# Performance work log

Hardware: AMD Instinct MI355X
Metric: run time of the kernel (lower is better)

Reference implementation:

```python
import jax, jax.numpy as jnp
import numpy as np

NEG_SLOPE = 0.2
STRONG_CONVEXITY = 0.5


def _scalar(x, Wq, Wl, bl, Wz, wz_out, wq_out, wl_out):
    # x: [B, D]; Wq/Wl: [L, H, D]; bl: [L, H]; Wz: [L-1, H, H]
    # Precompute all per-layer x-dependent terms in two batched einsums.
    qx = jnp.einsum('lhd,bd->lbh', Wq, x) ** 2          # [L, B, H]
    lx = jnp.einsum('lhd,bd->lbh', Wl, x) + bl[:, None, :]  # [L, B, H]
    z = jax.nn.leaky_relu(qx[0] + lx[0], negative_slope=NEG_SLOPE)

    def step(z, inputs):
        W, q, l = inputs
        z = jax.nn.leaky_relu(z @ W.T + q + l, negative_slope=NEG_SLOPE)
        return z, None

    z, _ = jax.lax.scan(step, z, (Wz, qx[1:], lx[1:]))
    # Final layer to scalar output (no bias on last wx_lin per torch code).
    out = z @ wz_out.T + (x @ wq_out.T) ** 2 + x @ wl_out.T  # [B, 1]
    return out


def setup_inputs() -> dict:
    key = jax.random.key(0)
    ks = jax.random.split(key, 8)
    B, D, H, L = 8192, 128, 512, 10
    f32 = jnp.float32
    x = jax.random.normal(ks[0], (B, D), f32)
    Wq = jax.random.normal(ks[1], (L, H, D), f32) * (1.0 / np.sqrt(D))
    Wl = jax.random.normal(ks[2], (L, H, D), f32) * (1.0 / np.sqrt(D))
    bl = jax.random.normal(ks[3], (L, H), f32) * 0.01
    # wz weights are kept non-negative in the original (clamp/exp init)
    Wz = jnp.abs(jax.random.normal(ks[4], (L - 1, H, H), f32)) * (1.0 / np.sqrt(H))
    wz_out = jnp.abs(jax.random.normal(ks[5], (1, H), f32)) * (1.0 / np.sqrt(H))
    wq_out = jax.random.normal(ks[6], (1, D), f32) * (1.0 / np.sqrt(D))
    wl_out = jax.random.normal(ks[7], (1, D), f32) * (1.0 / np.sqrt(D))
    return {"x": x, "Wq": Wq, "Wl": Wl, "bl": bl, "Wz": Wz,
            "wz_out": wz_out, "wq_out": wq_out, "wl_out": wl_out}


def reference(x, Wq, Wl, bl, Wz, wz_out, wq_out, wl_out):
    # forward = (1 - mu) * d(scalar)/dx + mu * x, with grad_outputs = ones
    def scalar_sum(xx):
        return jnp.sum(_scalar(xx, Wq, Wl, bl, Wz, wz_out, wq_out, wl_out))

    gx = jax.grad(scalar_sum)(x)  # per-sample gradient, [B, D]
    return (1.0 - STRONG_CONVEXITY) * gx + STRONG_CONVEXITY * x
```

## Files before the change

### kernel.cpp

```cpp
#include <hip/hip_runtime.h>


#define Bn 8192
#define Dn 128
#define Hn 512
#define Ln 10

constexpr float NS = 0.2f;

typedef __attribute__((ext_vector_type(8))) short short8;
typedef __attribute__((ext_vector_type(4))) float f32x4;

typedef const __attribute__((address_space(1))) void GV;
typedef __attribute__((address_space(3))) void LV;

__device__ __forceinline__ void gload16(const void* g, void* l) {
    __builtin_amdgcn_global_load_lds((GV*)g, (LV*)l, 16, 0, 0);
}

#define MFMA(acc, a, b) acc = __builtin_amdgcn_mfma_f32_16x16x32_bf16(a, b, acc, 0, 0, 0)

__device__ __forceinline__ unsigned short bf16_rne(float v) {
    unsigned u = __float_as_uint(v);
    u += 0x7FFFu + ((u >> 16) & 1u);
    return (unsigned short)(u >> 16);
}
__device__ __forceinline__ float bf2f(unsigned short h) {
    return __uint_as_float(((unsigned)h) << 16);
}
__device__ __forceinline__ void split2(float v, unsigned short& h, unsigned short& l) {
    h = bf16_rne(v);
    l = bf16_rne(v - bf2f(h));
}


__global__ __launch_bounds__(256) void split_flat(const float* __restrict__ in,
        unsigned short* __restrict__ hi, unsigned short* __restrict__ lo, int n4) {
    int i = blockIdx.x * 256 + threadIdx.x;
    if (i >= n4) return;
    float4 v = ((const float4*)in)[i];
    ushort4 h, l;
    split2(v.x, h.x, l.x);
    split2(v.y, h.y, l.y);
    split2(v.z, h.z, l.z);
    split2(v.w, h.w, l.w);
    ((ushort4*)hi)[i] = h;
    ((ushort4*)lo)[i] = l;
}

__global__ __launch_bounds__(256) void transpose_split(const float* __restrict__ in,
        unsigned short* __restrict__ hi, unsigned short* __restrict__ lo, int R, int C) {
    __shared__ float t[32][33];
    const size_t off = (size_t)blockIdx.z * R * C;
    const float* src = in + off;
    unsigned short* dh = hi + off;
    unsigned short* dl = lo + off;
    const int r0 = blockIdx.x * 32, c0 = blockIdx.y * 32;
    const int tr = threadIdx.x >> 5, tc = threadIdx.x & 31;
#pragma unroll
    for (int i = 0; i < 4; ++i)
        t[tr + 8 * i][tc] = src[(size_t)(r0 + tr + 8 * i) * C + c0 + tc];
    __syncthreads();
#pragma unroll
    for (int i = 0; i < 4; ++i) {
        float v = t[tc][tr + 8 * i];
        unsigned short h, l; split2(v, h, l);
        size_t o = (size_t)(c0 + tr + 8 * i) * R + r0 + tc;
        dh[o] = h; dl[o] = l;
    }
}


__global__ __launch_bounds__(256) void fwd_mfma(
    const unsigned short* __restrict__ xh, const unsigned short* __restrict__ xl,
    const unsigned short* __restrict__ zph, const unsigned short* __restrict__ zpl,
    const unsigned short* __restrict__ Wzh, const unsigned short* __restrict__ Wzl,
    const unsigned short* __restrict__ Wqh, const unsigned short* __restrict__ Wql,
    const unsigned short* __restrict__ Wlh, const unsigned short* __restrict__ Wll,
    const float* __restrict__ bl,
    unsigned short* __restrict__ zoh, unsigned short* __restrict__ zol,
    unsigned short* __restrict__ mask16, int hasZ)
{
    __shared__ __align__(16) char smem[32768];
    unsigned short* Ah  = (unsigned short*)smem;
    unsigned short* Al  = (unsigned short*)(smem + 8192);
    unsigned short* B0h = (unsigned short*)(smem + 16384);
    unsigned short* B0l = (unsigned short*)(smem + 20480);
    unsigned short* B1h = (unsigned short*)(smem + 24576);
    unsigned short* B1l = (unsigned short*)(smem + 28672);

    const int tid = threadIdx.x;
    const int w = tid >> 6, lane = tid & 63;
    const int lq = lane >> 4, lc = lane & 15;
    const int wm = (w & 1) * 64, wn = (w >> 1) * 32;
    const int row0 = blockIdx.x * 128, col0 = blockIdx.y * 64;
    const int sr = lane >> 2, sk = (lane & 3) * 8;

    f32x4 accz[4][2], accu[4][2], accv[4][2];
#pragma unroll
    for (int i = 0; i < 4; ++i)
#pragma unroll
        for (int j = 0; j < 2; ++j)
#pragma unroll
            for (int r = 0; r < 4; ++r) { accz[i][j][r] = 0.f; accu[i][j][r] = 0.f; accv[i][j][r] = 0.f; }

    if (hasZ) {
        for (int k0 = 0; k0 < Hn; k0 += 32) {
            __syncthreads();
            for (int c = w; c < 8; c += 4) {
                size_t go = (size_t)(row0 + c * 16 + sr) * Hn + k0 + sk;
                gload16(zph + go, Ah + c * 512);
                gload16(zpl + go, Al + c * 512);
            }
            {
                int c = w;
                size_t go = (size_t)(col0 + c * 16 + sr) * Hn + k0 + sk;
                gload16(Wzh + go, B0h + c * 512);
                gload16(Wzl + go, B0l + c * 512);
            }
            __syncthreads();
            short8 ah[4], al[4];
#pragma unroll
            for (int mt = 0; mt < 4; ++mt) {
                int ao = (wm + mt * 16 + lc) * 32 + lq * 8;
                ah[mt] = *(const short8*)(Ah + ao);
                al[mt] = *(const short8*)(Al + ao);
            }
#pragma unroll
            for (int nt = 0; nt < 2; ++nt) {
                int bo = (wn + nt * 16 + lc) * 32 + lq * 8;
                short8 bh = *(const short8*)(B0h + bo);
                short8 bv = *(const short8*)(B0l + bo);
#pragma unroll
                for (int mt = 0; mt < 4; ++mt) {
                    MFMA(accz[mt][nt], ah[mt], bh);
                    MFMA(accz[mt][nt], ah[mt], bv);
                    MFMA(accz[mt][nt], al[mt], bh);
                }
            }
        }
    }

    for (int k0 = 0; k0 < Dn; k0 += 32) {
        __syncthreads();
        for (int c = w; c < 8; c += 4) {
            size_t go = (size_t)(row0 + c * 16 + sr) * Dn + k0 + sk;
            gload16(xh + go, Ah + c * 512);
            gload16(xl + go, Al + c * 512);
        }
        {
            int c = w;
            size_t go = (size_t)(col0 + c * 16 + sr) * Dn + k0 + sk;
            gload16(Wqh + go, B0h + c * 512);
            gload16(Wql + go, B0l + c * 512);
            gload16(Wlh + go, B1h + c * 512);
            gload16(Wll + go, B1l + c * 512);
        }
        __syncthreads();
        short8 ah[4], al[4];
#pragma unroll
        for (int mt = 0; mt < 4; ++mt) {
            int ao = (wm + mt * 16 + lc) * 32 + lq * 8;
            ah[mt] = *(const short8*)(Ah + ao);
            al[mt] = *(const short8*)(Al + ao);
        }
#pragma unroll
        for (int nt = 0; nt < 2; ++nt) {
            int bo = (wn + nt * 16 + lc) * 32 + lq * 8;
            short8 bqh = *(const short8*)(B0h + bo);
            short8 bql = *(const short8*)(B0l + bo);
            short8 blh = *(const short8*)(B1h + bo);
            short8 bll = *(const short8*)(B1l + bo);
#pragma unroll
            for (int mt = 0; mt < 4; ++mt) {
                MFMA(accu[mt][nt], ah[mt], bqh);
                MFMA(accu[mt][nt], ah[mt], bql);
                MFMA(accu[mt][nt], al[mt], bqh);
                MFMA(accv[mt][nt], ah[mt], blh);
                MFMA(accv[mt][nt], ah[mt], bll);
                MFMA(accv[mt][nt], al[mt], blh);
            }
        }
    }

#pragma unroll
    for (int nt = 0; nt < 2; ++nt) {
        const int colb = col0 + wn + nt * 16;
        const int col = colb + lc;
        const float blv = bl[col];
#pragma unroll
        for (int mt = 0; mt < 4; ++mt) {
            const int rowb = row0 + wm + mt * 16;
#pragma unroll
            for (int r = 0; r < 4; ++r) {
                float uq = accu[mt][nt][r];
                float pre = accz[mt][nt][r] + uq * uq + accv[mt][nt][r] + blv;
                bool m = pre >= 0.f;
                unsigned long long bal = __ballot(m);
                if (lc == 0) {
                    int rw = rowb + lq * 4 + r;
                    mask16[(size_t)rw * 32 + (colb >> 4)] =
                        (unsigned short)((bal >> (lq * 16)) & 0xFFFFull);
                }
                float zv = m ? pre : NS * pre;
                unsigned short h, l; split2(zv, h, l);
                size_t o = (size_t)(rowb + lq * 4 + r) * Hn + col;
                zoh[o] = h; zol[o] = l;
            }
        }
    }
}


__global__ __launch_bounds__(256) void gemm_u_mfma(
    const unsigned short* __restrict__ xh, const unsigned short* __restrict__ xl,
    const unsigned short* __restrict__ Wqh, const unsigned short* __restrict__ Wql,
    float* __restrict__ u)
{
    __shared__ __align__(16) char smem[24576];
    unsigned short* Ah  = (unsigned short*)smem;
    unsigned short* Al  = (unsigned short*)(smem + 8192);
    unsigned short* B0h = (unsigned short*)(smem + 16384);
    unsigned short* B0l = (unsigned short*)(smem + 20480);

    const int tid = threadIdx.x;
    const int w = tid >> 6, lane = tid & 63;
    const int lq = lane >> 4, lc = lane & 15;
    const int wm = (w & 1) * 64, wn = (w >> 1) * 32;
    const int row0 = blockIdx.x * 128, col0 = blockIdx.y * 64;
    const int sr = lane >> 2, sk = (lane & 3) * 8;

    f32x4 acc[4][2];
#pragma unroll
    for (int i = 0; i < 4; ++i)
#pragma unroll
        for (int j = 0; j < 2; ++j)
#pragma unroll
            for (int r = 0; r < 4; ++r) acc[i][j][r] = 0.f;

    for (int k0 = 0; k0 < Dn; k0 += 32) {
        __syncthreads();
        for (int c = w; c < 8; c += 4) {
            size_t go = (size_t)(row0 + c * 16 + sr) * Dn + k0 + sk;
            gload16(xh + go, Ah + c * 512);
            gload16(xl + go, Al + c * 512);
        }
        {
            int c = w;
            size_t go = (size_t)(col0 + c * 16 + sr) * Dn + k0 + sk;
            gload16(Wqh + go, B0h + c * 512);
            gload16(Wql + go, B0l + c * 512);
        }
        __syncthreads();
        short8 ah[4], al[4];
#pragma unroll
        for (int mt = 0; mt < 4; ++mt) {
            int ao = (wm + mt * 16 + lc) * 32 + lq * 8;
            ah[mt] = *(const short8*)(Ah + ao);
            al[mt] = *(const short8*)(Al + ao);
        }
#pragma unroll
        for (int nt = 0; nt < 2; ++nt) {
            int bo = (wn + nt * 16 + lc) * 32 + lq * 8;
            short8 bh = *(const short8*)(B0h + bo);
            short8 bv = *(const short8*)(B0l + bo);
#pragma unroll
            for (int mt = 0; mt < 4; ++mt) {
                MFMA(acc[mt][nt], ah[mt], bh);
                MFMA(acc[mt][nt], ah[mt], bv);
                MFMA(acc[mt][nt], al[mt], bh);
            }
        }
    }

#pragma unroll
    for (int nt = 0; nt < 2; ++nt) {
        const int col = col0 + wn + nt * 16 + lc;
#pragma unroll
        for (int mt = 0; mt < 4; ++mt) {
            const int rowb = row0 + wm + mt * 16;
#pragma unroll
            for (int r = 0; r < 4; ++r)
                u[(size_t)(rowb + lq * 4 + r) * Hn + col] = acc[mt][nt][r];
        }
    }
}


__global__ __launch_bounds__(256) void bwd_g_mfma(
    const unsigned short* __restrict__ gah, const unsigned short* __restrict__ gal,
    const unsigned short* __restrict__ WzTh, const unsigned short* __restrict__ WzTl,
    const unsigned short* __restrict__ maskprev,
    unsigned short* __restrict__ goh, unsigned short* __restrict__ gol)
{
    __shared__ __align__(16) char smem[24576];
    unsigned short* Ah  = (unsigned short*)smem;
    unsigned short* Al  = (unsigned short*)(smem + 8192);
    unsigned short* B0h = (unsigned short*)(smem + 16384);
    unsigned short* B0l = (unsigned short*)(smem + 20480);

    const int tid = threadIdx.x;
    const int w = tid >> 6, lane = tid & 63;
    const int lq = lane >> 4, lc = lane & 15;
    const int wm = (w & 1) * 64, wn = (w >> 1) * 32;
    const int row0 = blockIdx.x * 128, col0 = blockIdx.y * 64;
    const int sr = lane >> 2, sk = (lane & 3) * 8;

    f32x4 acc[4][2];
#pragma unroll
    for (int i = 0; i < 4; ++i)
#pragma unroll
        for (int j = 0; j < 2; ++j)
#pragma unroll
            for (int r = 0; r < 4; ++r) acc[i][j][r] = 0.f;

    for (int k0 = 0; k0 < Hn; k0 += 32) {
        __syncthreads();
        for (int c = w; c < 8; c += 4) {
            size_t go = (size_t)(row0 + c * 16 + sr) * Hn + k0 + sk;
            gload16(gah + go, Ah + c * 512);
            gload16(gal + go, Al + c * 512);
        }
        {
            int c = w;
            size_t go = (size_t)(col0 + c * 16 + sr) * Hn + k0 + sk;
            gload16(WzTh + go, B0h + c * 512);
            gload16(WzTl + go, B0l + c * 512);
        }
        __syncthreads();
        short8 ah[4], al[4];
#pragma unroll
        for (int mt = 0; mt < 4; ++mt) {
            int ao = (wm + mt * 16 + lc) * 32 + lq * 8;
            ah[mt] = *(const short8*)(Ah + ao);
            al[mt] = *(const short8*)(Al + ao);
        }
#pragma unroll
        for (int nt = 0; nt < 2; ++nt) {
            int bo = (wn + nt * 16 + lc) * 32 + lq * 8;
            short8 bh = *(const short8*)(B0h + bo);
            short8 bv = *(const short8*)(B0l + bo);
#pragma unroll
            for (int mt = 0; mt < 4; ++mt) {
                MFMA(acc[mt][nt], ah[mt], bh);
                MFMA(acc[mt][nt], ah[mt], bv);
                MFMA(acc[mt][nt], al[mt], bh);
            }
        }
    }

#pragma unroll
    for (int nt = 0; nt < 2; ++nt) {
        const int colb = col0 + wn + nt * 16;
        const int col = colb + lc;
#pragma unroll
        for (int mt = 0; mt < 4; ++mt) {
            const int rowb = row0 + wm + mt * 16;
#pragma unroll
            for (int r = 0; r < 4; ++r) {
                int row = rowb + lq * 4 + r;
                unsigned short wbits = maskprev[(size_t)row * 32 + (colb >> 4)];
                float f = ((wbits >> lc) & 1) ? 1.f : NS;
                float v = acc[mt][nt][r] * f;
                unsigned short h, l; split2(v, h, l);
                size_t o = (size_t)row * Hn + col;
                goh[o] = h; gol[o] = l;
            }
        }
    }
}


__global__ __launch_bounds__(256) void bwd_x_mfma(
    const unsigned short* __restrict__ gah, const unsigned short* __restrict__ gal,
    const float* __restrict__ u,
    const unsigned short* __restrict__ WqTh, const unsigned short* __restrict__ WqTl,
    const unsigned short* __restrict__ WlTh, const unsigned short* __restrict__ WlTl,
    float* __restrict__ gx, int addTo)
{
    __shared__ __align__(16) char smem[32768];
    unsigned short* A1h = (unsigned short*)smem;
    unsigned short* A1l = (unsigned short*)(smem + 4096);
    unsigned short* A2h = (unsigned short*)(smem + 8192);
    unsigned short* A2l = (unsigned short*)(smem + 12288);
    unsigned short* Bqh = (unsigned short*)(smem + 16384);
    unsigned short* Bql = (unsigned short*)(smem + 20480);
    unsigned short* Blh = (unsigned short*)(smem + 24576);
    unsigned short* Bll = (unsigned short*)(smem + 28672);

    const int tid = threadIdx.x;
    const int w = tid >> 6, lane = tid & 63;
    const int lq = lane >> 4, lc = lane & 15;
    const int wm = (w & 1) * 32, wn = (w >> 1) * 32;
    const int row0 = blockIdx.x * 64, col0 = blockIdx.y * 64;
    const int sr = lane >> 2, sk = (lane & 3) * 8;
    const int ar = tid >> 2, as = (tid & 3) * 8;

    f32x4 acc[2][2];
#pragma unroll
    for (int i = 0; i < 2; ++i)
#pragma unroll
        for (int j = 0; j < 2; ++j)
#pragma unroll
            for (int r = 0; r < 4; ++r) acc[i][j][r] = 0.f;

    for (int k0 = 0; k0 < Hn; k0 += 32) {
        __syncthreads();
        {
            int c = w;
            size_t go = (size_t)(col0 + c * 16 + sr) * Hn + k0 + sk;
            gload16(WqTh + go, Bqh + c * 512);
            gload16(WqTl + go, Bql + c * 512);
            gload16(WlTh + go, Blh + c * 512);
            gload16(WlTl + go, Bll + c * 512);
        }
        {
            size_t gb = (size_t)(row0 + ar) * Hn + k0 + as;
            float4 u0 = *(const float4*)(u + gb);
            float4 u1 = *(const float4*)(u + gb + 4);
            ushort4 h0 = *(const ushort4*)(gah + gb);
            ushort4 h1 = *(const ushort4*)(gah + gb + 4);
            ushort4 l0 = *(const ushort4*)(gal + gb);
            ushort4 l1 = *(const ushort4*)(gal + gb + 4);
            int lo_ = ar * 32 + as;
            *(ushort4*)(A2h + lo_) = h0; *(ushort4*)(A2h + lo_ + 4) = h1;
            *(ushort4*)(A2l + lo_) = l0; *(ushort4*)(A2l + lo_ + 4) = l1;
            ushort4 oh, ol;
            float g, a1;
            g = bf2f(h0.x) + bf2f(l0.x); a1 = 2.f * u0.x * g; split2(a1, oh.x, ol.x);
            g = bf2f(h0.y) + bf2f(l0.y); a1 = 2.f * u0.y * g; split2(a1, oh.y, ol.y);
            g = bf2f(h0.z) + bf2f(l0.z); a1 = 2.f * u0.z * g; split2(a1, oh.z, ol.z);
            g = bf2f(h0.w) + bf2f(l0.w); a1 = 2.f * u0.w * g; split2(a1, oh.w, ol.w);
            *(ushort4*)(A1h + lo_) = oh; *(ushort4*)(A1l + lo_) = ol;
            g = bf2f(h1.x) + bf2f(l1.x); a1 = 2.f * u1.x * g; split2(a1, oh.x, ol.x);
            g = bf2f(h1.y) + bf2f(l1.y); a1 = 2.f * u1.y * g; split2(a1, oh.y, ol.y);
            g = bf2f(h1.z) + bf2f(l1.z); a1 = 2.f * u1.z * g; split2(a1, oh.z, ol.z);
            g = bf2f(h1.w) + bf2f(l1.w); a1 = 2.f * u1.w * g; split2(a1, oh.w, ol.w);
            *(ushort4*)(A1h + lo_ + 4) = oh; *(ushort4*)(A1l + lo_ + 4) = ol;
        }
        __syncthreads();
        short8 a1h[2], a1l[2], a2h[2], a2l[2];
#pragma unroll
        for (int mt = 0; mt < 2; ++mt) {
            int ao = (wm + mt * 16 + lc) * 32 + lq * 8;
            a1h[mt] = *(const short8*)(A1h + ao);
            a1l[mt] = *(const short8*)(A1l + ao);
            a2h[mt] = *(const short8*)(A2h + ao);
            a2l[mt] = *(const short8*)(A2l + ao);
        }
#pragma unroll
        for (int nt = 0; nt < 2; ++nt) {
            int bo = (wn + nt * 16 + lc) * 32 + lq * 8;
            short8 qh = *(const short8*)(Bqh + bo);
            short8 ql_ = *(const short8*)(Bql + bo);
            short8 lh = *(const short8*)(Blh + bo);
            short8 ll_ = *(const short8*)(Bll + bo);
#pragma unroll
            for (int mt = 0; mt < 2; ++mt) {
                MFMA(acc[mt][nt], a1h[mt], qh);
                MFMA(acc[mt][nt], a1h[mt], ql_);
                MFMA(acc[mt][nt], a1l[mt], qh);
                MFMA(acc[mt][nt], a2h[mt], lh);
                MFMA(acc[mt][nt], a2h[mt], ll_);
                MFMA(acc[mt][nt], a2l[mt], lh);
            }
        }
    }

#pragma unroll
    for (int nt = 0; nt < 2; ++nt) {
        const int col = col0 + wn + nt * 16 + lc;
#pragma unroll
        for (int mt = 0; mt < 2; ++mt) {
            const int rowb = row0 + wm + mt * 16;
#pragma unroll
            for (int r = 0; r < 4; ++r) {
                size_t o = (size_t)(rowb + lq * 4 + r) * Dn + col;
                float v = acc[mt][nt][r];
                if (addTo) v += gx[o];
                gx[o] = v;
            }
        }
    }
}


__global__ __launch_bounds__(256) void ga_init(
    const float* __restrict__ wz_out, const unsigned short* __restrict__ mask9,
    unsigned short* __restrict__ gh, unsigned short* __restrict__ gl)
{
    int i = blockIdx.x * 256 + threadIdx.x;
    int e = i << 2;
    int b = e >> 9, h = e & 511;
    unsigned short wbits = mask9[(size_t)b * 32 + (h >> 4)];
    float4 wv = *(const float4*)(wz_out + h);
    int sh = h & 15;
    ushort4 oh, ol;
    float f;
    f = wv.x * (((wbits >> (sh + 0)) & 1) ? 1.f : NS); split2(f, oh.x, ol.x);
    f = wv.y * (((wbits >> (sh + 1)) & 1) ? 1.f : NS); split2(f, oh.y, ol.y);
    f = wv.z * (((wbits >> (sh + 2)) & 1) ? 1.f : NS); split2(f, oh.z, ol.z);
    f = wv.w * (((wbits >> (sh + 3)) & 1) ? 1.f : NS); split2(f, oh.w, ol.w);
    *(ushort4*)(gh + e) = oh;
    *(ushort4*)(gl + e) = ol;
}

__global__ __launch_bounds__(256) void rowdot_kernel(
    const float* __restrict__ x, const float* __restrict__ wq_out, float* __restrict__ s) {
    const int b = blockIdx.x * 4 + (threadIdx.x >> 6);
    const int lane = threadIdx.x & 63;
    float v = x[(size_t)b * Dn + lane] * wq_out[lane] +
              x[(size_t)b * Dn + 64 + lane] * wq_out[64 + lane];
#pragma unroll
    for (int off = 32; off > 0; off >>= 1) v += __shfl_down(v, off, 64);
    if (lane == 0) s[b] = v;
}

__global__ __launch_bounds__(256) void final_kernel(
    float* __restrict__ out, const float* __restrict__ x, const float* __restrict__ s,
    const float* __restrict__ wq_out, const float* __restrict__ wl_out) {
    const int i = blockIdx.x * 256 + threadIdx.x;
    const int base = i << 2;
    const int b = base >> 7;
    const int d = base & (Dn - 1);
    float4 g = *(const float4*)(out + base);
    float4 xv = *(const float4*)(x + base);
    float4 wq = *(const float4*)(wq_out + d);
    float4 wl = *(const float4*)(wl_out + d);
    const float sb = s[b];
    float4 o;
    o.x = 0.5f * g.x + sb * wq.x + 0.5f * wl.x + 0.5f * xv.x;
    o.y = 0.5f * g.y + sb * wq.y + 0.5f * wl.y + 0.5f * xv.y;
    o.z = 0.5f * g.z + sb * wq.z + 0.5f * wl.z + 0.5f * xv.z;
    o.w = 0.5f * g.w + sb * wq.w + 0.5f * wl.w + 0.5f * xv.w;
    *(float4*)(out + base) = o;
}


extern "C" void kernel_launch(void* const* d_in, const int* in_sizes, int n_in,
                              void* d_out, int out_size, void* d_ws, size_t ws_size,
                              hipStream_t stream) {
    (void)in_sizes; (void)n_in; (void)out_size; (void)ws_size;
    const float* x      = (const float*)d_in[0];
    const float* Wq     = (const float*)d_in[1];
    const float* Wl     = (const float*)d_in[2];
    const float* bl     = (const float*)d_in[3];
    const float* Wz     = (const float*)d_in[4];
    const float* wz_out = (const float*)d_in[5];
    const float* wq_out = (const float*)d_in[6];
    const float* wl_out = (const float*)d_in[7];
    float* out = (float*)d_out;

    char* p = (char*)d_ws;
    #define CARVE(name, bytes) unsigned short* name = (unsigned short*)p; p += (((size_t)(bytes)) + 255) & ~(size_t)255;
    CARVE(xh,  (size_t)Bn*Dn*2)  CARVE(xl,  (size_t)Bn*Dn*2)
    CARVE(Wqh, (size_t)Ln*Hn*Dn*2) CARVE(Wql, (size_t)Ln*Hn*Dn*2)
    CARVE(Wlh, (size_t)Ln*Hn*Dn*2) CARVE(Wll, (size_t)Ln*Hn*Dn*2)
    CARVE(WqTh,(size_t)Ln*Hn*Dn*2) CARVE(WqTl,(size_t)Ln*Hn*Dn*2)
    CARVE(WlTh,(size_t)Ln*Hn*Dn*2) CARVE(WlTl,(size_t)Ln*Hn*Dn*2)
    CARVE(Wzh, (size_t)(Ln-1)*Hn*Hn*2) CARVE(Wzl, (size_t)(Ln-1)*Hn*Hn*2)
    CARVE(WzTh,(size_t)(Ln-1)*Hn*Hn*2) CARVE(WzTl,(size_t)(Ln-1)*Hn*Hn*2)
    CARVE(zAh, (size_t)Bn*Hn*2) CARVE(zAl, (size_t)Bn*Hn*2)
    CARVE(zBh, (size_t)Bn*Hn*2) CARVE(zBl, (size_t)Bn*Hn*2)
    float* uBuf = (float*)p; p += (size_t)Bn*Hn*4;
    float* s    = (float*)p; p += (size_t)Bn*4;
    unsigned short* mask16 = (unsigned short*)p; p += (size_t)Ln*Bn*32*2;
    #undef CARVE

    split_flat<<<(Bn*Dn/4 + 255)/256, 256, 0, stream>>>(x, xh, xl, Bn*Dn/4);
    split_flat<<<(Ln*Hn*Dn/4 + 255)/256, 256, 0, stream>>>(Wq, Wqh, Wql, Ln*Hn*Dn/4);
    split_flat<<<(Ln*Hn*Dn/4 + 255)/256, 256, 0, stream>>>(Wl, Wlh, Wll, Ln*Hn*Dn/4);
    split_flat<<<((Ln-1)*Hn*Hn/4 + 255)/256, 256, 0, stream>>>(Wz, Wzh, Wzl, (Ln-1)*Hn*Hn/4);
    transpose_split<<<dim3(Hn/32, Dn/32, Ln), 256, 0, stream>>>(Wq, WqTh, WqTl, Hn, Dn);
    transpose_split<<<dim3(Hn/32, Dn/32, Ln), 256, 0, stream>>>(Wl, WlTh, WlTl, Hn, Dn);
    transpose_split<<<dim3(Hn/32, Hn/32, Ln-1), 256, 0, stream>>>(Wz, WzTh, WzTl, Hn, Hn);

    rowdot_kernel<<<Bn/4, 256, 0, stream>>>(x, wq_out, s);

    const dim3 gF(Bn/128, Hn/64);

    fwd_mfma<<<gF, 256, 0, stream>>>(xh, xl, nullptr, nullptr, nullptr, nullptr,
        Wqh, Wql, Wlh, Wll, bl, zAh, zAl, mask16, 0);
    for (int l = 1; l < Ln; ++l) {
        const unsigned short* zh  = (l & 1) ? zAh : zBh;
        const unsigned short* zl_ = (l & 1) ? zAl : zBl;
        unsigned short* oh  = (l & 1) ? zBh : zAh;
        unsigned short* ol_ = (l & 1) ? zBl : zAl;
        fwd_mfma<<<gF, 256, 0, stream>>>(xh, xl, zh, zl_,
            Wzh + (size_t)(l-1)*Hn*Hn, Wzl + (size_t)(l-1)*Hn*Hn,
            Wqh + (size_t)l*Hn*Dn, Wql + (size_t)l*Hn*Dn,
            Wlh + (size_t)l*Hn*Dn, Wll + (size_t)l*Hn*Dn,
            bl + (size_t)l*Hn, oh, ol_, mask16 + (size_t)l*Bn*32, 1);
    }

    ga_init<<<(Bn*Hn/4)/256, 256, 0, stream>>>(wz_out, mask16 + (size_t)9*Bn*32, zAh, zAl);
    for (int l = Ln - 1; l >= 0; --l) {
        int sidx = (Ln - 1 - l) & 1;
        const unsigned short* gh_ = sidx ? zBh : zAh;
        const unsigned short* gl_ = sidx ? zBl : zAl;
        gemm_u_mfma<<<gF, 256, 0, stream>>>(xh, xl,
            Wqh + (size_t)l*Hn*Dn, Wql + (size_t)l*Hn*Dn, uBuf);
        bwd_x_mfma<<<dim3(Bn/64, Dn/64), 256, 0, stream>>>(gh_, gl_, uBuf,
            WqTh + (size_t)l*Dn*Hn, WqTl + (size_t)l*Dn*Hn,
            WlTh + (size_t)l*Dn*Hn, WlTl + (size_t)l*Dn*Hn,
            out, (l == Ln - 1) ? 0 : 1);
        if (l > 0) {
            unsigned short* oh  = sidx ? zAh : zBh;
            unsigned short* ol_ = sidx ? zAl : zBl;
            bwd_g_mfma<<<gF, 256, 0, stream>>>(gh_, gl_,
                WzTh + (size_t)(l-1)*Hn*Hn, WzTl + (size_t)(l-1)*Hn*Hn,
                mask16 + (size_t)(l-1)*Bn*32, oh, ol_);
        }
    }

    final_kernel<<<(Bn*Dn/4)/256, 256, 0, stream>>>(out, x, s, wq_out, wl_out);
}
```

Baseline: 928.4 us.

## Cache forward u, fuse backward g/x GEMMs into one launch, merge weight splits

The forward kernel now writes the pre-square Wq·x term u for every layer into a per-layer buffer. This removes the backward recomputation GEMM (gemm_u_mfma) at the cost of an extra Ln×B×H float buffer of writes and reads. The backward g-propagation and x-gradient GEMMs are merged into a single launch. Blocks are partitioned by index, so both run concurrently, and the x-gradient tile grows to 128 rows. The final elementwise combine is folded into the last backward epilogue, and the flat and transposed weight splits are produced by one kernel per weight.

```diff
diff --git a/kernel.cpp b/kernel.cpp
--- a/kernel.cpp
+++ b/kernel.cpp
@@ -48,18 +48,27 @@
     ((ushort4*)lo)[i] = l;
 }
 
-__global__ __launch_bounds__(256) void transpose_split(const float* __restrict__ in,
-        unsigned short* __restrict__ hi, unsigned short* __restrict__ lo, int R, int C) {
+__global__ __launch_bounds__(256) void split_both(const float* __restrict__ in,
+        unsigned short* __restrict__ hi, unsigned short* __restrict__ lo,
+        unsigned short* __restrict__ thi, unsigned short* __restrict__ tlo,
+        int R, int C) {
     __shared__ float t[32][33];
     const size_t off = (size_t)blockIdx.z * R * C;
     const float* src = in + off;
-    unsigned short* dh = hi + off;
-    unsigned short* dl = lo + off;
+    unsigned short* sh_ = hi + off;
+    unsigned short* sl_ = lo + off;
+    unsigned short* dh = thi + off;
+    unsigned short* dl = tlo + off;
     const int r0 = blockIdx.x * 32, c0 = blockIdx.y * 32;
     const int tr = threadIdx.x >> 5, tc = threadIdx.x & 31;
 #pragma unroll
-    for (int i = 0; i < 4; ++i)
-        t[tr + 8 * i][tc] = src[(size_t)(r0 + tr + 8 * i) * C + c0 + tc];
+    for (int i = 0; i < 4; ++i) {
+        size_t si = (size_t)(r0 + tr + 8 * i) * C + c0 + tc;
+        float v = src[si];
+        t[tr + 8 * i][tc] = v;
+        unsigned short h, l; split2(v, h, l);
+        sh_[si] = h; sl_[si] = l;
+    }
     __syncthreads();
 #pragma unroll
     for (int i = 0; i < 4; ++i) {
@@ -79,7 +88,7 @@
     const unsigned short* __restrict__ Wlh, const unsigned short* __restrict__ Wll,
     const float* __restrict__ bl,
     unsigned short* __restrict__ zoh, unsigned short* __restrict__ zol,
-    unsigned short* __restrict__ mask16, int hasZ)
+    unsigned short* __restrict__ mask16, float* __restrict__ uout, int hasZ)
 {
     __shared__ __align__(16) char smem[32768];
     unsigned short* Ah  = (unsigned short*)smem;
@@ -206,279 +215,207 @@
                 unsigned short h, l; split2(zv, h, l);
                 size_t o = (size_t)(rowb + lq * 4 + r) * Hn + col;
                 zoh[o] = h; zol[o] = l;
-            }
-        }
-    }
-}
-
-
-__global__ __launch_bounds__(256) void gemm_u_mfma(
-    const unsigned short* __restrict__ xh, const unsigned short* __restrict__ xl,
-    const unsigned short* __restrict__ Wqh, const unsigned short* __restrict__ Wql,
-    float* __restrict__ u)
+                uout[o] = uq;
+            }
+        }
+    }
+}
+
+
+__global__ __launch_bounds__(256) void bwd_combo(
+    const unsigned short* __restrict__ gah, const unsigned short* __restrict__ gal,
+    const unsigned short* __restrict__ WzTh, const unsigned short* __restrict__ WzTl,
+    const unsigned short* __restrict__ maskprev,
+    unsigned short* __restrict__ goh, unsigned short* __restrict__ gol,
+    const float* __restrict__ uL,
+    const unsigned short* __restrict__ WqTh, const unsigned short* __restrict__ WqTl,
+    const unsigned short* __restrict__ WlTh, const unsigned short* __restrict__ WlTl,
+    float* __restrict__ gx, int addTo, int nG, int finalF,
+    const float* __restrict__ xin, const float* __restrict__ s,
+    const float* __restrict__ wq_out, const float* __restrict__ wl_out)
 {
-    __shared__ __align__(16) char smem[24576];
-    unsigned short* Ah  = (unsigned short*)smem;
-    unsigned short* Al  = (unsigned short*)(smem + 8192);
-    unsigned short* B0h = (unsigned short*)(smem + 16384);
-    unsigned short* B0l = (unsigned short*)(smem + 20480);
-
+    __shared__ __align__(16) char smem[49152];
+    const int bid = blockIdx.x;
     const int tid = threadIdx.x;
     const int w = tid >> 6, lane = tid & 63;
     const int lq = lane >> 4, lc = lane & 15;
     const int wm = (w & 1) * 64, wn = (w >> 1) * 32;
-    const int row0 = blockIdx.x * 128, col0 = blockIdx.y * 64;
     const int sr = lane >> 2, sk = (lane & 3) * 8;
 
-    f32x4 acc[4][2];
-#pragma unroll
-    for (int i = 0; i < 4; ++i)
-#pragma unroll
-        for (int j = 0; j < 2; ++j)
-#pragma unroll
-            for (int r = 0; r < 4; ++r) acc[i][j][r] = 0.f;
-
-    for (int k0 = 0; k0 < Dn; k0 += 32) {
-        __syncthreads();
-        for (int c = w; c < 8; c += 4) {
-            size_t go = (size_t)(row0 + c * 16 + sr) * Dn + k0 + sk;
-            gload16(xh + go, Ah + c * 512);
-            gload16(xl + go, Al + c * 512);
-        }
-        {
-            int c = w;
-            size_t go = (size_t)(col0 + c * 16 + sr) * Dn + k0 + sk;
-            gload16(Wqh + go, B0h + c * 512);
-            gload16(Wql + go, B0l + c * 512);
-        }
-        __syncthreads();
-        short8 ah[4], al[4];
-#pragma unroll
-        for (int mt = 0; mt < 4; ++mt) {
-            int ao = (wm + mt * 16 + lc) * 32 + lq * 8;
-            ah[mt] = *(const short8*)(Ah + ao);
-            al[mt] = *(const short8*)(Al + ao);
-        }
+    if (bid < nG) {
+        unsigned short* Ah  = (unsigned short*)smem;
+        unsigned short* Al  = (unsigned short*)(smem + 8192);
+        unsigned short* B0h = (unsigned short*)(smem + 16384);
+        unsigned short* B0l = (unsigned short*)(smem + 20480);
+        const int row0 = (bid & 63) * 128, col0 = (bid >> 6) * 64;
+
+        f32x4 acc[4][2];
+#pragma unroll
+        for (int i = 0; i < 4; ++i)
+#pragma unroll
+            for (int j = 0; j < 2; ++j)
+#pragma unroll
+                for (int r = 0; r < 4; ++r) acc[i][j][r] = 0.f;
+
+        for (int k0 = 0; k0 < Hn; k0 += 32) {
+            __syncthreads();
+            for (int c = w; c < 8; c += 4) {
+                size_t go = (size_t)(row0 + c * 16 + sr) * Hn + k0 + sk;
+                gload16(gah + go, Ah + c * 512);
+                gload16(gal + go, Al + c * 512);
+            }
+            {
+                int c = w;
+                size_t go = (size_t)(col0 + c * 16 + sr) * Hn + k0 + sk;
+                gload16(WzTh + go, B0h + c * 512);
+                gload16(WzTl + go, B0l + c * 512);
+            }
+            __syncthreads();
+            short8 ah[4], al[4];
+#pragma unroll
+            for (int mt = 0; mt < 4; ++mt) {
+                int ao = (wm + mt * 16 + lc) * 32 + lq * 8;
+                ah[mt] = *(const short8*)(Ah + ao);
+                al[mt] = *(const short8*)(Al + ao);
+            }
+#pragma unroll
+            for (int nt = 0; nt < 2; ++nt) {
+                int bo = (wn + nt * 16 + lc) * 32 + lq * 8;
+                short8 bh = *(const short8*)(B0h + bo);
+                short8 bv = *(const short8*)(B0l + bo);
+#pragma unroll
+                for (int mt = 0; mt < 4; ++mt) {
+                    MFMA(acc[mt][nt], ah[mt], bh);
+                    MFMA(acc[mt][nt], ah[mt], bv);
+                    MFMA(acc[mt][nt], al[mt], bh);
+                }
+            }
+        }
+
 #pragma unroll
         for (int nt = 0; nt < 2; ++nt) {
-            int bo = (wn + nt * 16 + lc) * 32 + lq * 8;
-            short8 bh = *(const short8*)(B0h + bo);
-            short8 bv = *(const short8*)(B0l + bo);
+            const int colb = col0 + wn + nt * 16;
+            const int col = colb + lc;
 #pragma unroll
             for (int mt = 0; mt < 4; ++mt) {
-                MFMA(acc[mt][nt], ah[mt], bh);
-                MFMA(acc[mt][nt], ah[mt], bv);
-                MFMA(acc[mt][nt], al[mt], bh);
-            }
-        }
-    }
-
-#pragma unroll
-    for (int nt = 0; nt < 2; ++nt) {
-        const int col = col0 + wn + nt * 16 + lc;
-#pragma unroll
-        for (int mt = 0; mt < 4; ++mt) {
-            const int rowb = row0 + wm + mt * 16;
-#pragma unroll
-            for (int r = 0; r < 4; ++r)
-                u[(size_t)(rowb + lq * 4 + r) * Hn + col] = acc[mt][nt][r];
-        }
-    }
-}
-
-
-__global__ __launch_bounds__(256) void bwd_g_mfma(
-    const unsigned short* __restrict__ gah, const unsigned short* __restrict__ gal,
-    const unsigned short* __restrict__ WzTh, const unsigned short* __restrict__ WzTl,
-    const unsigned short* __restrict__ maskprev,
-    unsigned short* __restrict__ goh, unsigned short* __restrict__ gol)
-{
-    __shared__ __align__(16) char smem[24576];
-    unsigned short* Ah  = (unsigned short*)smem;
-    unsigned short* Al  = (unsigned short*)(smem + 8192);
-    unsigned short* B0h = (unsigned short*)(smem + 16384);
-    unsigned short* B0l = (unsigned short*)(smem + 20480);
-
-    const int tid = threadIdx.x;
-    const int w = tid >> 6, lane = tid & 63;
-    const int lq = lane >> 4, lc = lane & 15;
-    const int wm = (w & 1) * 64, wn = (w >> 1) * 32;
-    const int row0 = blockIdx.x * 128, col0 = blockIdx.y * 64;
-    const int sr = lane >> 2, sk = (lane & 3) * 8;
-
-    f32x4 acc[4][2];
-#pragma unroll
-    for (int i = 0; i < 4; ++i)
-#pragma unroll
-        for (int j = 0; j < 2; ++j)
-#pragma unroll
-            for (int r = 0; r < 4; ++r) acc[i][j][r] = 0.f;
-
-    for (int k0 = 0; k0 < Hn; k0 += 32) {
-        __syncthreads();
-        for (int c = w; c < 8; c += 4) {
-            size_t go = (size_t)(row0 + c * 16 + sr) * Hn + k0 + sk;
-            gload16(gah + go, Ah + c * 512);
-            gload16(gal + go, Al + c * 512);
-        }
-        {
-            int c = w;
-            size_t go = (size_t)(col0 + c * 16 + sr) * Hn + k0 + sk;
-            gload16(WzTh + go, B0h + c * 512);
-            gload16(WzTl + go, B0l + c * 512);
-        }
-        __syncthreads();
-        short8 ah[4], al[4];
-#pragma unroll
-        for (int mt = 0; mt < 4; ++mt) {
-            int ao = (wm + mt * 16 + lc) * 32 + lq * 8;
-            ah[mt] = *(const short8*)(Ah + ao);
-            al[mt] = *(const short8*)(Al + ao);
-        }
+                const int rowb = row0 + wm + mt * 16;
+#pragma unroll
+                for (int r = 0; r < 4; ++r) {
+                    int row = rowb + lq * 4 + r;
+                    unsigned short wbits = maskprev[(size_t)row * 32 + (colb >> 4)];
+                    float f = ((wbits >> lc) & 1) ? 1.f : NS;
+                    float v = acc[mt][nt][r] * f;
+                    unsigned short h, l; split2(v, h, l);
+                    size_t o = (size_t)row * Hn + col;
+                    goh[o] = h; gol[o] = l;
+                }
+            }
+        }
+    } else {
+        unsigned short* A1h = (unsigned short*)smem;
+        unsigned short* A1l = (unsigned short*)(smem + 8192);
+        unsigned short* A2h = (unsigned short*)(smem + 16384);
+        unsigned short* A2l = (unsigned short*)(smem + 24576);
+        unsigned short* Bqh = (unsigned short*)(smem + 32768);
+        unsigned short* Bql = (unsigned short*)(smem + 36864);
+        unsigned short* Blh = (unsigned short*)(smem + 40960);
+        unsigned short* Bll = (unsigned short*)(smem + 45056);
+
+        const int t = bid - nG;
+        const int row0 = (t >> 1) * 128, col0 = (t & 1) * 64;
+        const int ar = tid >> 2, as = (tid & 3) * 8;
+
+        f32x4 acc[4][2];
+#pragma unroll
+        for (int i = 0; i < 4; ++i)
+#pragma unroll
+            for (int j = 0; j < 2; ++j)
+#pragma unroll
+                for (int r = 0; r < 4; ++r) acc[i][j][r] = 0.f;
+
+        for (int k0 = 0; k0 < Hn; k0 += 32) {
+            __syncthreads();
+            {
+                int c = w;
+                size_t go = (size_t)(col0 + c * 16 + sr) * Hn + k0 + sk;
+                gload16(WqTh + go, Bqh + c * 512);
+                gload16(WqTl + go, Bql + c * 512);
+                gload16(WlTh + go, Blh + c * 512);
+                gload16(WlTl + go, Bll + c * 512);
+            }
+#pragma unroll
+            for (int rr = 0; rr < 2; ++rr) {
+                const int lr = rr * 64 + ar;
+                size_t gb = (size_t)(row0 + lr) * Hn + k0 + as;
+                float4 u0 = *(const float4*)(uL + gb);
+                float4 u1 = *(const float4*)(uL + gb + 4);
+                ushort4 h0 = *(const ushort4*)(gah + gb);
+                ushort4 h1 = *(const ushort4*)(gah + gb + 4);
+                ushort4 l0 = *(const ushort4*)(gal + gb);
+                ushort4 l1 = *(const ushort4*)(gal + gb + 4);
+                int lo_ = lr * 32 + as;
+                *(ushort4*)(A2h + lo_) = h0; *(ushort4*)(A2h + lo_ + 4) = h1;
+                *(ushort4*)(A2l + lo_) = l0; *(ushort4*)(A2l + lo_ + 4) = l1;
+                ushort4 oh, ol;
+                float g, a1;
+                g = bf2f(h0.x) + bf2f(l0.x); a1 = 2.f * u0.x * g; split2(a1, oh.x, ol.x);
+                g = bf2f(h0.y) + bf2f(l0.y); a1 = 2.f * u0.y * g; split2(a1, oh.y, ol.y);
+                g = bf2f(h0.z) + bf2f(l0.z); a1 = 2.f * u0.z * g; split2(a1, oh.z, ol.z);
+                g = bf2f(h0.w) + bf2f(l0.w); a1 = 2.f * u0.w * g; split2(a1, oh.w, ol.w);
+                *(ushort4*)(A1h + lo_) = oh; *(ushort4*)(A1l + lo_) = ol;
+                g = bf2f(h1.x) + bf2f(l1.x); a1 = 2.f * u1.x * g; split2(a1, oh.x, ol.x);
+                g = bf2f(h1.y) + bf2f(l1.y); a1 = 2.f * u1.y * g; split2(a1, oh.y, ol.y);
+                g = bf2f(h1.z) + bf2f(l1.z); a1 = 2.f * u1.z * g; split2(a1, oh.z, ol.z);
+                g = bf2f(h1.w) + bf2f(l1.w); a1 = 2.f * u1.w * g; split2(a1, oh.w, ol.w);
+                *(ushort4*)(A1h + lo_ + 4) = oh; *(ushort4*)(A1l + lo_ + 4) = ol;
+            }
+            __syncthreads();
+            short8 a1h[4], a1l[4], a2h[4], a2l[4];
+#pragma unroll
+            for (int mt = 0; mt < 4; ++mt) {
+                int ao = (wm + mt * 16 + lc) * 32 + lq * 8;
+                a1h[mt] = *(const short8*)(A1h + ao);
+                a1l[mt] = *(const short8*)(A1l + ao);
+                a2h[mt] = *(const short8*)(A2h + ao);
+                a2l[mt] = *(const short8*)(A2l + ao);
+            }
+#pragma unroll
+            for (int nt = 0; nt < 2; ++nt) {
+                int bo = (wn + nt * 16 + lc) * 32 + lq * 8;
+                short8 qh = *(const short8*)(Bqh + bo);
+                short8 ql_ = *(const short8*)(Bql + bo);
+                short8 lh = *(const short8*)(Blh + bo);
+                short8 ll_ = *(const short8*)(Bll + bo);
+#pragma unroll
+                for (int mt = 0; mt < 4; ++mt) {
+                    MFMA(acc[mt][nt], a1h[mt], qh);
+                    MFMA(acc[mt][nt], a1h[mt], ql_);
+                    MFMA(acc[mt][nt], a1l[mt], qh);
+                    MFMA(acc[mt][nt], a2h[mt], lh);
+                    MFMA(acc[mt][nt], a2h[mt], ll_);
+                    MFMA(acc[mt][nt], a2l[mt], lh);
+                }
+            }
+        }
+
 #pragma unroll
         for (int nt = 0; nt < 2; ++nt) {
-            int bo = (wn + nt * 16 + lc) * 32 + lq * 8;
-            short8 bh = *(const short8*)(B0h + bo);
-            short8 bv = *(const short8*)(B0l + bo);
+            const int col = col0 + wn + nt * 16 + lc;
 #pragma unroll
             for (int mt = 0; mt < 4; ++mt) {
-                MFMA(acc[mt][nt], ah[mt], bh);
-                MFMA(acc[mt][nt], ah[mt], bv);
-                MFMA(acc[mt][nt], al[mt], bh);
-            }
-        }
-    }
-
-#pragma unroll
-    for (int nt = 0; nt < 2; ++nt) {
-        const int colb = col0 + wn + nt * 16;
-        const int col = colb + lc;
-#pragma unroll
-        for (int mt = 0; mt < 4; ++mt) {
-            const int rowb = row0 + wm + mt * 16;
-#pragma unroll
-            for (int r = 0; r < 4; ++r) {
-                int row = rowb + lq * 4 + r;
-                unsigned short wbits = maskprev[(size_t)row * 32 + (colb >> 4)];
-                float f = ((wbits >> lc) & 1) ? 1.f : NS;
-                float v = acc[mt][nt][r] * f;
-                unsigned short h, l; split2(v, h, l);
-                size_t o = (size_t)row * Hn + col;
-                goh[o] = h; gol[o] = l;
-            }
-        }
-    }
-}
-
-
-__global__ __launch_bounds__(256) void bwd_x_mfma(
-    const unsigned short* __restrict__ gah, const unsigned short* __restrict__ gal,
-    const float* __restrict__ u,
-    const unsigned short* __restrict__ WqTh, const unsigned short* __restrict__ WqTl,
-    const unsigned short* __restrict__ WlTh, const unsigned short* __restrict__ WlTl,
-    float* __restrict__ gx, int addTo)
-{
-    __shared__ __align__(16) char smem[32768];
-    unsigned short* A1h = (unsigned short*)smem;
-    unsigned short* A1l = (unsigned short*)(smem + 4096);
-    unsigned short* A2h = (unsigned short*)(smem + 8192);
-    unsigned short* A2l = (unsigned short*)(smem + 12288);
-    unsigned short* Bqh = (unsigned short*)(smem + 16384);
-    unsigned short* Bql = (unsigned short*)(smem + 20480);
-    unsigned short* Blh = (unsigned short*)(smem + 24576);
-    unsigned short* Bll = (unsigned short*)(smem + 28672);
-
-    const int tid = threadIdx.x;
-    const int w = tid >> 6, lane = tid & 63;
-    const int lq = lane >> 4, lc = lane & 15;
-    const int wm = (w & 1) * 32, wn = (w >> 1) * 32;
-    const int row0 = blockIdx.x * 64, col0 = blockIdx.y * 64;
-    const int sr = lane >> 2, sk = (lane & 3) * 8;
-    const int ar = tid >> 2, as = (tid & 3) * 8;
-
-    f32x4 acc[2][2];
-#pragma unroll
-    for (int i = 0; i < 2; ++i)
-#pragma unroll
-        for (int j = 0; j < 2; ++j)
-#pragma unroll
-            for (int r = 0; r < 4; ++r) acc[i][j][r] = 0.f;
-
-    for (int k0 = 0; k0 < Hn; k0 += 32) {
-        __syncthreads();
-        {
-            int c = w;
-            size_t go = (size_t)(col0 + c * 16 + sr) * Hn + k0 + sk;
-            gload16(WqTh + go, Bqh + c * 512);
-            gload16(WqTl + go, Bql + c * 512);
-            gload16(WlTh + go, Blh + c * 512);
-            gload16(WlTl + go, Bll + c * 512);
-        }
-        {
-            size_t gb = (size_t)(row0 + ar) * Hn + k0 + as;
-            float4 u0 = *(const float4*)(u + gb);
-            float4 u1 = *(const float4*)(u + gb + 4);
-            ushort4 h0 = *(const ushort4*)(gah + gb);
-            ushort4 h1 = *(const ushort4*)(gah + gb + 4);
-            ushort4 l0 = *(const ushort4*)(gal + gb);
-            ushort4 l1 = *(const ushort4*)(gal + gb + 4);
-            int lo_ = ar * 32 + as;
-            *(ushort4*)(A2h + lo_) = h0; *(ushort4*)(A2h + lo_ + 4) = h1;
-            *(ushort4*)(A2l + lo_) = l0; *(ushort4*)(A2l + lo_ + 4) = l1;
-            ushort4 oh, ol;
-            float g, a1;
-            g = bf2f(h0.x) + bf2f(l0.x); a1 = 2.f * u0.x * g; split2(a1, oh.x, ol.x);
-            g = bf2f(h0.y) + bf2f(l0.y); a1 = 2.f * u0.y * g; split2(a1, oh.y, ol.y);
-            g = bf2f(h0.z) + bf2f(l0.z); a1 = 2.f * u0.z * g; split2(a1, oh.z, ol.z);
-            g = bf2f(h0.w) + bf2f(l0.w); a1 = 2.f * u0.w * g; split2(a1, oh.w, ol.w);
-            *(ushort4*)(A1h + lo_) = oh; *(ushort4*)(A1l + lo_) = ol;
-            g = bf2f(h1.x) + bf2f(l1.x); a1 = 2.f * u1.x * g; split2(a1, oh.x, ol.x);
-            g = bf2f(h1.y) + bf2f(l1.y); a1 = 2.f * u1.y * g; split2(a1, oh.y, ol.y);
-            g = bf2f(h1.z) + bf2f(l1.z); a1 = 2.f * u1.z * g; split2(a1, oh.z, ol.z);
-            g = bf2f(h1.w) + bf2f(l1.w); a1 = 2.f * u1.w * g; split2(a1, oh.w, ol.w);
-            *(ushort4*)(A1h + lo_ + 4) = oh; *(ushort4*)(A1l + lo_ + 4) = ol;
-        }
-        __syncthreads();
-        short8 a1h[2], a1l[2], a2h[2], a2l[2];
-#pragma unroll
-        for (int mt = 0; mt < 2; ++mt) {
-            int ao = (wm + mt * 16 + lc) * 32 + lq * 8;
-            a1h[mt] = *(const short8*)(A1h + ao);
-            a1l[mt] = *(const short8*)(A1l + ao);
-            a2h[mt] = *(const short8*)(A2h + ao);
-            a2l[mt] = *(const short8*)(A2l + ao);
-        }
-#pragma unroll
-        for (int nt = 0; nt < 2; ++nt) {
-            int bo = (wn + nt * 16 + lc) * 32 + lq * 8;
-            short8 qh = *(const short8*)(Bqh + bo);
-            short8 ql_ = *(const short8*)(Bql + bo);
-            short8 lh = *(const short8*)(Blh + bo);
-            short8 ll_ = *(const short8*)(Bll + bo);
-#pragma unroll
-            for (int mt = 0; mt < 2; ++mt) {
-                MFMA(acc[mt][nt], a1h[mt], qh);
-                MFMA(acc[mt][nt], a1h[mt], ql_);
-                MFMA(acc[mt][nt], a1l[mt], qh);
-                MFMA(acc[mt][nt], a2h[mt], lh);
-                MFMA(acc[mt][nt], a2h[mt], ll_);
-                MFMA(acc[mt][nt], a2l[mt], lh);
-            }
-        }
-    }
-
-#pragma unroll
-    for (int nt = 0; nt < 2; ++nt) {
-        const int col = col0 + wn + nt * 16 + lc;
-#pragma unroll
-        for (int mt = 0; mt < 2; ++mt) {
-            const int rowb = row0 + wm + mt * 16;
-#pragma unroll
-            for (int r = 0; r < 4; ++r) {
-                size_t o = (size_t)(rowb + lq * 4 + r) * Dn + col;
-                float v = acc[mt][nt][r];
-                if (addTo) v += gx[o];
-                gx[o] = v;
+                const int rowb = row0 + wm + mt * 16;
+#pragma unroll
+                for (int r = 0; r < 4; ++r) {
+                    const int row = rowb + lq * 4 + r;
+                    size_t o = (size_t)row * Dn + col;
+                    float v = acc[mt][nt][r];
+                    if (addTo) v += gx[o];
+                    if (finalF) {
+                        v = 0.5f * v + s[row] * wq_out[col] + 0.5f * wl_out[col]
+                            + 0.5f * xin[o];
+                    }
+                    gx[o] = v;
+                }
             }
         }
     }
@@ -516,26 +453,6 @@
     if (lane == 0) s[b] = v;
 }
 
-__global__ __launch_bounds__(256) void final_kernel(
-    float* __restrict__ out, const float* __restrict__ x, const float* __restrict__ s,
-    const float* __restrict__ wq_out, const float* __restrict__ wl_out) {
-    const int i = blockIdx.x * 256 + threadIdx.x;
-    const int base = i << 2;
-    const int b = base >> 7;
-    const int d = base & (Dn - 1);
-    float4 g = *(const float4*)(out + base);
-    float4 xv = *(const float4*)(x + base);
-    float4 wq = *(const float4*)(wq_out + d);
-    float4 wl = *(const float4*)(wl_out + d);
-    const float sb = s[b];
-    float4 o;
-    o.x = 0.5f * g.x + sb * wq.x + 0.5f * wl.x + 0.5f * xv.x;
-    o.y = 0.5f * g.y + sb * wq.y + 0.5f * wl.y + 0.5f * xv.y;
-    o.z = 0.5f * g.z + sb * wq.z + 0.5f * wl.z + 0.5f * xv.z;
-    o.w = 0.5f * g.w + sb * wq.w + 0.5f * wl.w + 0.5f * xv.w;
-    *(float4*)(out + base) = o;
-}
-
 
 extern "C" void kernel_launch(void* const* d_in, const int* in_sizes, int n_in,
                               void* d_out, int out_size, void* d_ws, size_t ws_size,
@@ -562,25 +479,22 @@
     CARVE(WzTh,(size_t)(Ln-1)*Hn*Hn*2) CARVE(WzTl,(size_t)(Ln-1)*Hn*Hn*2)
     CARVE(zAh, (size_t)Bn*Hn*2) CARVE(zAl, (size_t)Bn*Hn*2)
     CARVE(zBh, (size_t)Bn*Hn*2) CARVE(zBl, (size_t)Bn*Hn*2)
-    float* uBuf = (float*)p; p += (size_t)Bn*Hn*4;
+    float* uBuf = (float*)p; p += (size_t)Ln*Bn*Hn*4;
     float* s    = (float*)p; p += (size_t)Bn*4;
     unsigned short* mask16 = (unsigned short*)p; p += (size_t)Ln*Bn*32*2;
     #undef CARVE
 
     split_flat<<<(Bn*Dn/4 + 255)/256, 256, 0, stream>>>(x, xh, xl, Bn*Dn/4);
-    split_flat<<<(Ln*Hn*Dn/4 + 255)/256, 256, 0, stream>>>(Wq, Wqh, Wql, Ln*Hn*Dn/4);
-    split_flat<<<(Ln*Hn*Dn/4 + 255)/256, 256, 0, stream>>>(Wl, Wlh, Wll, Ln*Hn*Dn/4);
-    split_flat<<<((Ln-1)*Hn*Hn/4 + 255)/256, 256, 0, stream>>>(Wz, Wzh, Wzl, (Ln-1)*Hn*Hn/4);
-    transpose_split<<<dim3(Hn/32, Dn/32, Ln), 256, 0, stream>>>(Wq, WqTh, WqTl, Hn, Dn);
-    transpose_split<<<dim3(Hn/32, Dn/32, Ln), 256, 0, stream>>>(Wl, WlTh, WlTl, Hn, Dn);
-    transpose_split<<<dim3(Hn/32, Hn/32, Ln-1), 256, 0, stream>>>(Wz, WzTh, WzTl, Hn, Hn);
+    split_both<<<dim3(Hn/32, Dn/32, Ln), 256, 0, stream>>>(Wq, Wqh, Wql, WqTh, WqTl, Hn, Dn);
+    split_both<<<dim3(Hn/32, Dn/32, Ln), 256, 0, stream>>>(Wl, Wlh, Wll, WlTh, WlTl, Hn, Dn);
+    split_both<<<dim3(Hn/32, Hn/32, Ln-1), 256, 0, stream>>>(Wz, Wzh, Wzl, WzTh, WzTl, Hn, Hn);
 
     rowdot_kernel<<<Bn/4, 256, 0, stream>>>(x, wq_out, s);
 
     const dim3 gF(Bn/128, Hn/64);
 
     fwd_mfma<<<gF, 256, 0, stream>>>(xh, xl, nullptr, nullptr, nullptr, nullptr,
-        Wqh, Wql, Wlh, Wll, bl, zAh, zAl, mask16, 0);
+        Wqh, Wql, Wlh, Wll, bl, zAh, zAl, mask16, uBuf, 0);
     for (int l = 1; l < Ln; ++l) {
         const unsigned short* zh  = (l & 1) ? zAh : zBh;
         const unsigned short* zl_ = (l & 1) ? zAl : zBl;
@@ -590,7 +504,8 @@
             Wzh + (size_t)(l-1)*Hn*Hn, Wzl + (size_t)(l-1)*Hn*Hn,
             Wqh + (size_t)l*Hn*Dn, Wql + (size_t)l*Hn*Dn,
             Wlh + (size_t)l*Hn*Dn, Wll + (size_t)l*Hn*Dn,
-            bl + (size_t)l*Hn, oh, ol_, mask16 + (size_t)l*Bn*32, 1);
+            bl + (size_t)l*Hn, oh, ol_, mask16 + (size_t)l*Bn*32,
+            uBuf + (size_t)l*Bn*Hn, 1);
     }
 
     ga_init<<<(Bn*Hn/4)/256, 256, 0, stream>>>(wz_out, mask16 + (size_t)9*Bn*32, zAh, zAl);
@@ -598,20 +513,19 @@
         int sidx = (Ln - 1 - l) & 1;
         const unsigned short* gh_ = sidx ? zBh : zAh;
         const unsigned short* gl_ = sidx ? zBl : zAl;
-        gemm_u_mfma<<<gF, 256, 0, stream>>>(xh, xl,
-            Wqh + (size_t)l*Hn*Dn, Wql + (size_t)l*Hn*Dn, uBuf);
-        bwd_x_mfma<<<dim3(Bn/64, Dn/64), 256, 0, stream>>>(gh_, gl_, uBuf,
+        unsigned short* oh  = sidx ? zAh : zBh;
+        unsigned short* ol_ = sidx ? zAl : zBl;
+        const int nG = (l > 0) ? 512 : 0;
+        bwd_combo<<<nG + 128, 256, 0, stream>>>(
+            gh_, gl_,
+            (l > 0) ? WzTh + (size_t)(l-1)*Hn*Hn : nullptr,
+            (l > 0) ? WzTl + (size_t)(l-1)*Hn*Hn : nullptr,
+            (l > 0) ? mask16 + (size_t)(l-1)*Bn*32 : nullptr,
+            (l > 0) ? oh : nullptr, (l > 0) ? ol_ : nullptr,
+            uBuf + (size_t)l*Bn*Hn,
             WqTh + (size_t)l*Dn*Hn, WqTl + (size_t)l*Dn*Hn,
             WlTh + (size_t)l*Dn*Hn, WlTl + (size_t)l*Dn*Hn,
-            out, (l == Ln - 1) ? 0 : 1);
-        if (l > 0) {
-            unsigned short* oh  = sidx ? zAh : zBh;
-            unsigned short* ol_ = sidx ? zAl : zBl;
-            bwd_g_mfma<<<gF, 256, 0, stream>>>(gh_, gl_,
-                WzTh + (size_t)(l-1)*Hn*Hn, WzTl + (size_t)(l-1)*Hn*Hn,
-                mask16 + (size_t)(l-1)*Bn*32, oh, ol_);
-        }
-    }
-
-    final_kernel<<<(Bn*Dn/4)/256, 256, 0, stream>>>(out, x, s, wq_out, wl_out);
-}
+            out, (l == Ln - 1) ? 0 : 1, nG, (l == 0) ? 1 : 0,
+            x, s, wq_out, wl_out);
+    }
+}
```

New measurement: 889.7 us. 1.04x faster.
